# Optimization experiments

Hardware: AMD Instinct MI355X
Metric: run time of the kernel (lower is better)

The kernel has to match this reference:

```python
import jax, jax.numpy as jnp
import numpy as np

EPS = 2.220446049250313e-16  # np.finfo(float).eps, used by SparseDispatcher.combine


def setup_inputs() -> dict:
    key = jax.random.key(0)
    k1, k2, k3, k4, k5, k6 = jax.random.split(key, 6)
    N, D, H, E = 16384, 512, 2048, 8
    x = jax.random.normal(k1, (N, D), dtype=jnp.float32)
    w_gate = jax.random.normal(k2, (D, E), dtype=jnp.float32) * 0.05
    W1 = jax.random.normal(k3, (E - 1, D, H), dtype=jnp.float32) * 0.02
    b1 = jax.random.normal(k4, (E - 1, H), dtype=jnp.float32) * 0.02
    W2 = jax.random.normal(k5, (E - 1, H, D), dtype=jnp.float32) * 0.02
    b2 = jax.random.normal(k6, (E - 1, D), dtype=jnp.float32) * 0.02
    return {"x": x, "w_gate": w_gate, "W1": W1, "b1": b1, "W2": W2, "b2": b2, "k": 2}


def reference(x, w_gate, W1, b1, W2, b2, k):
    # --- top-k gating (input_choice, node-level, no noise / eval mode) ---
    N, E = x.shape[0], w_gate.shape[1]
    logits = x @ w_gate                                   # [N, E]
    top_vals, top_idx = jax.lax.top_k(logits, k)          # [N, k]
    top_gates = jax.nn.softmax(top_vals, axis=-1)         # softmax over selected experts
    gates = jnp.zeros((N, E), x.dtype).at[jnp.arange(N)[:, None], top_idx].set(top_gates)
    # --- dispatch / per-expert MLP / weighted combine ---
    # output[b] = sum_i gates[b,i] * expert_i(x[b]); last expert is identity.
    out = gates[:, E - 1 : E] * x                         # IdentityExpert (expert E-1)
    for e in range(W1.shape[0]):                          # fixed small expert count
        h = jax.nn.relu(x @ W1[e] + b1[e])                # [N, H]
        out = out + gates[:, e : e + 1] * (h @ W2[e] + b2[e])
    out = out.astype(jnp.float32)
    # combine() replaces exact zeros with machine epsilon
    return jnp.where(out == 0, EPS, out)
```

## Files before the change

### kernel.cpp

```cpp
#include <hip/hip_runtime.h>
#include <stdint.h>

#define EPS_VAL 2.220446049250313e-16f

typedef unsigned short u16;
typedef __bf16 bf16x8 __attribute__((ext_vector_type(8)));
typedef float f32x4 __attribute__((ext_vector_type(4)));

static __device__ __forceinline__ u16 f2bf(float v) {
    __bf16 b = (__bf16)v;
    return __builtin_bit_cast(u16, b);
}
static __device__ __forceinline__ float bf2f(u16 u) {
    __bf16 b = __builtin_bit_cast(__bf16, u);
    return (float)b;
}
static __device__ __forceinline__ void gll16(const void* g, void* l) {
    __builtin_amdgcn_global_load_lds(
        (const __attribute__((address_space(1))) unsigned int*)g,
        (__attribute__((address_space(3))) unsigned int*)l, 16, 0, 0);
}

#define MT_CAP 40

__global__ void k_transpose_cvt(const float* __restrict__ in, u16* __restrict__ out,
                                int R, int C) {
    __shared__ float t[32][33];
    const float* ip = in + (size_t)blockIdx.z * R * C;
    u16* op = out + (size_t)blockIdx.z * R * C;
    int tx = threadIdx.x & 31, ty = threadIdx.x >> 5;
    int c = blockIdx.x * 32 + tx;
    #pragma unroll
    for (int i = 0; i < 4; ++i) {
        int r = blockIdx.y * 32 + ty + i * 8;
        t[ty + i * 8][tx] = ip[(size_t)r * C + c];
    }
    __syncthreads();
    int r2 = blockIdx.y * 32 + tx;
    #pragma unroll
    for (int i = 0; i < 4; ++i) {
        int c2 = blockIdx.x * 32 + ty + i * 8;
        op[(size_t)c2 * R + r2] = f2bf(t[tx][ty + i * 8]);
    }
}

__global__ __launch_bounds__(1024) void k_gate(
    const float* __restrict__ x, const float* __restrict__ wg,
    u16* __restrict__ xb, int* __restrict__ cnt,
    uint2* __restrict__ asg, float4* __restrict__ rec) {
    __shared__ int hist[8];
    __shared__ int basep[8];
    __shared__ int   eA[64], eB[64], rA[64], rB[64];
    __shared__ float gA[64], gB[64];

    const int tid = threadIdx.x;
    if (tid < 8) hist[tid] = 0;
    __syncthreads();

    const int wv = tid >> 6, lane = tid & 63;
    #pragma unroll
    for (int it = 0; it < 4; ++it) {
        int rl  = it * 16 + wv;
        int row = blockIdx.x * 64 + rl;
        const float4* px = (const float4*)(x + (size_t)row * 512) + lane * 2;
        float4 v0 = px[0], v1 = px[1];
        union { u16 h[8]; uint4 u; } o;
        o.h[0]=f2bf(v0.x); o.h[1]=f2bf(v0.y); o.h[2]=f2bf(v0.z); o.h[3]=f2bf(v0.w);
        o.h[4]=f2bf(v1.x); o.h[5]=f2bf(v1.y); o.h[6]=f2bf(v1.z); o.h[7]=f2bf(v1.w);
        ((uint4*)(xb + (size_t)row * 512))[lane] = o.u;

        float xv[8] = {v0.x, v0.y, v0.z, v0.w, v1.x, v1.y, v1.z, v1.w};
        float a0=0,a1=0,a2=0,a3=0,a4=0,a5=0,a6=0,a7=0;
        const float4* wp = (const float4*)wg + (size_t)lane * 16;
        #pragma unroll
        for (int j = 0; j < 8; ++j) {
            float4 wa = wp[j * 2], wb = wp[j * 2 + 1];
            float v = xv[j];
            a0 += v*wa.x; a1 += v*wa.y; a2 += v*wa.z; a3 += v*wa.w;
            a4 += v*wb.x; a5 += v*wb.y; a6 += v*wb.z; a7 += v*wb.w;
        }
        #pragma unroll
        for (int off = 32; off; off >>= 1) {
            a0 += __shfl_xor(a0, off); a1 += __shfl_xor(a1, off);
            a2 += __shfl_xor(a2, off); a3 += __shfl_xor(a3, off);
            a4 += __shfl_xor(a4, off); a5 += __shfl_xor(a5, off);
            a6 += __shfl_xor(a6, off); a7 += __shfl_xor(a7, off);
        }
        if (lane == 0) {
            float v[8] = {a0,a1,a2,a3,a4,a5,a6,a7};
            int i0 = 0;
            #pragma unroll
            for (int e = 1; e < 8; ++e) if (v[e] > v[i0]) i0 = e;
            int i1 = (i0 == 0) ? 1 : 0;
            #pragma unroll
            for (int e = 0; e < 8; ++e) if (e != i0 && v[e] > v[i1]) i1 = e;
            float ex = expf(v[i1] - v[i0]);
            float g0 = 1.f / (1.f + ex), g1 = ex / (1.f + ex);
            rec[row] = make_float4(__int_as_float(i0), __int_as_float(i1), g0, g1);
            int r0 = (i0 != 7) ? atomicAdd(&hist[i0], 1) : -1;
            int r1 = (i1 != 7) ? atomicAdd(&hist[i1], 1) : -1;
            eA[rl] = i0; eB[rl] = i1; rA[rl] = r0; rB[rl] = r1;
            gA[rl] = g0; gB[rl] = g1;
        }
    }
    __syncthreads();
    if (tid < 7) basep[tid] = atomicAdd(&cnt[tid], hist[tid]);
    __syncthreads();
    if (tid < 64) {
        int row = blockIdx.x * 64 + tid;
        int i0 = eA[tid], i1 = eB[tid];
        if (i0 != 7)
            asg[i0 * 16384 + basep[i0] + rA[tid]] =
                make_uint2((unsigned)(row << 1), __float_as_uint(gA[tid]));
        if (i1 != 7)
            asg[i1 * 16384 + basep[i1] + rB[tid]] =
                make_uint2((unsigned)((row << 1) | 1), __float_as_uint(gB[tid]));
    }
}

__global__ void k_prefix(const int* __restrict__ cnt, int* __restrict__ off) {
    if (threadIdx.x == 0) {
        int s = 0;
        for (int e = 0; e < 7; ++e) { off[e] = s; s += cnt[e]; }
        off[7] = s;
    }
}

__global__ __launch_bounds__(256) void k_e1(
    const u16* __restrict__ xb, const u16* __restrict__ w1t,
    const float* __restrict__ b1, const int* __restrict__ cnt,
    const int* __restrict__ off, const uint2* __restrict__ asg,
    u16* __restrict__ Hb, int h0, int S, int NT)
{
    __shared__ __attribute__((aligned(16))) char smem[40960];

    const int bid = blockIdx.x;
    const int t   = (bid & 7) * (35 * NT) + (bid >> 3);
    const int e   = t / (MT_CAP * NT);
    const int rem = t - e * (MT_CAP * NT);
    const int mt  = rem / NT;
    const int nt  = rem - mt * NT;

    const int ce  = cnt[e];
    const int mtb = mt * 128;
    if (mtb >= ce) return;
    const int ntb = nt * 128;

    const int tid = threadIdx.x, wv = tid >> 6, lane = tid & 63;
    const int l16 = lane & 15, q = lane >> 4;
    const int wr = wv >> 1, wc = wv & 1;
    const u16* w1p = w1t + (size_t)e * 2048 * 512;

    const int nj = (wv < 2) ? 3 : 2;
    const u16* aS[3]; const u16* bS[3]; int js[3];
    #pragma unroll
    for (int jj = 0; jj < 3; ++jj) {
        int j = wv + jj * 4; js[jj] = j;
        if (j < 10) {
            int g = j * 64 + lane, row = g / 5, sl = g % 5;
            if (sl == 4) sl = 0;
            int idx = mtb + row;
            int rs = 0;
            if (idx < ce) rs = (int)asg[e * 16384 + idx].x >> 1;
            aS[jj] = xb + (size_t)rs * 512 + sl * 8;
            bS[jj] = w1p + (size_t)(h0 + ntb + row) * 512 + sl * 8;
        } else { aS[jj] = xb; bS[jj] = w1p; }
    }

    #pragma unroll
    for (int jj = 0; jj < 3; ++jj) if (jj < nj) {
        gll16(aS[jj], smem + js[jj] * 1024);
        gll16(bS[jj], smem + 20480 + js[jj] * 1024);
    }
    __syncthreads();

    f32x4 acc[4][4];
    #pragma unroll
    for (int mti = 0; mti < 4; ++mti)
        #pragma unroll
        for (int nti = 0; nti < 4; ++nti) acc[mti][nti] = (f32x4){0.f, 0.f, 0.f, 0.f};

    for (int kt = 0; kt < 16; ++kt) {
        const int cur = kt & 1;
        if (kt < 15) {
            char* An = smem + (cur ^ 1) * 10240;
            char* Bn = smem + 20480 + (cur ^ 1) * 10240;
            int ko = (kt + 1) * 32;
            #pragma unroll
            for (int jj = 0; jj < 3; ++jj) if (jj < nj) {
                gll16(aS[jj] + ko, An + js[jj] * 1024);
                gll16(bS[jj] + ko, Bn + js[jj] * 1024);
            }
        }
        const char* Ab = smem + cur * 10240;
        const char* Bb = smem + 20480 + cur * 10240;
        bf16x8 af[4], bf[4];
        #pragma unroll
        for (int mti = 0; mti < 4; ++mti)
            af[mti] = *(const bf16x8*)(Ab + (wr * 64 + mti * 16 + l16) * 80 + q * 16);
        #pragma unroll
        for (int nti = 0; nti < 4; ++nti)
            bf[nti] = *(const bf16x8*)(Bb + (wc * 64 + nti * 16 + l16) * 80 + q * 16);
        #pragma unroll
        for (int mti = 0; mti < 4; ++mti)
            #pragma unroll
            for (int nti = 0; nti < 4; ++nti)
                acc[mti][nti] = __builtin_amdgcn_mfma_f32_16x16x32_bf16(
                    af[mti], bf[nti], acc[mti][nti], 0, 0, 0);
        __syncthreads();
    }

    const size_t hbase = (size_t)off[e];
    #pragma unroll
    for (int nti = 0; nti < 4; ++nti) {
        int hcol = ntb + wc * 64 + nti * 16 + l16;
        float bias = b1[e * 2048 + h0 + hcol];
        #pragma unroll
        for (int mti = 0; mti < 4; ++mti) {
            #pragma unroll
            for (int r = 0; r < 4; ++r) {
                int i = mtb + wr * 64 + mti * 16 + q * 4 + r;
                if (i < ce) {
                    float v = acc[mti][nti][r] + bias;
                    v = v > 0.f ? v : 0.f;
                    Hb[(hbase + i) * S + hcol] = f2bf(v);
                }
            }
        }
    }
}

__global__ __launch_bounds__(256) void k_e2(
    const u16* __restrict__ Hb, const u16* __restrict__ w2t,
    const float* __restrict__ b2, const int* __restrict__ cnt,
    const int* __restrict__ off, const uint2* __restrict__ asg,
    u16* __restrict__ ybuf, int h0, int S, int firstPass, int lastPass)
{
    __shared__ __attribute__((aligned(16))) char smem[40960];

    const int bid = blockIdx.x;
    const int t   = (bid & 7) * 140 + (bid >> 3);
    const int e   = t / (MT_CAP * 4);
    const int rem = t - e * (MT_CAP * 4);
    const int mt  = rem >> 2;
    const int dt  = rem & 3;

    const int ce  = cnt[e];
    const int mtb = mt * 128;
    if (mtb >= ce) return;
    const int dtb = dt * 128;

    const int tid = threadIdx.x, wv = tid >> 6, lane = tid & 63;
    const int l16 = lane & 15, q = lane >> 4;
    const int wr = wv >> 1, wc = wv & 1;
    const u16* w2p = w2t + (size_t)e * 512 * 2048;
    const size_t hbase = (size_t)off[e];

    const int nj = (wv < 2) ? 3 : 2;
    const u16* aS[3]; const u16* bS[3]; int js[3];
    #pragma unroll
    for (int jj = 0; jj < 3; ++jj) {
        int j = wv + jj * 4; js[jj] = j;
        if (j < 10) {
            int g = j * 64 + lane, row = g / 5, sl = g % 5;
            if (sl == 4) sl = 0;
            aS[jj] = Hb + (hbase + mtb + row) * S + sl * 8;
            bS[jj] = w2p + (size_t)(dtb + row) * 2048 + h0 + sl * 8;
        } else { aS[jj] = Hb; bS[jj] = w2p; }
    }

    #pragma unroll
    for (int jj = 0; jj < 3; ++jj) if (jj < nj) {
        gll16(aS[jj], smem + js[jj] * 1024);
        gll16(bS[jj], smem + 20480 + js[jj] * 1024);
    }
    __syncthreads();

    f32x4 acc[4][4];
    #pragma unroll
    for (int mti = 0; mti < 4; ++mti)
        #pragma unroll
        for (int nti = 0; nti < 4; ++nti) acc[mti][nti] = (f32x4){0.f, 0.f, 0.f, 0.f};

    const int KT = S >> 5;
    for (int kt = 0; kt < KT; ++kt) {
        const int cur = kt & 1;
        if (kt + 1 < KT) {
            char* An = smem + (cur ^ 1) * 10240;
            char* Bn = smem + 20480 + (cur ^ 1) * 10240;
            int ko = (kt + 1) * 32;
            #pragma unroll
            for (int jj = 0; jj < 3; ++jj) if (jj < nj) {
                gll16(aS[jj] + ko, An + js[jj] * 1024);
                gll16(bS[jj] + ko, Bn + js[jj] * 1024);
            }
        }
        const char* Ab = smem + cur * 10240;
        const char* Bb = smem + 20480 + cur * 10240;
        bf16x8 af[4], bf[4];
        #pragma unroll
        for (int mti = 0; mti < 4; ++mti)
            af[mti] = *(const bf16x8*)(Ab + (wr * 64 + mti * 16 + l16) * 80 + q * 16);
        #pragma unroll
        for (int nti = 0; nti < 4; ++nti)
            bf[nti] = *(const bf16x8*)(Bb + (wc * 64 + nti * 16 + l16) * 80 + q * 16);
        #pragma unroll
        for (int mti = 0; mti < 4; ++mti)
            #pragma unroll
            for (int nti = 0; nti < 4; ++nti)
                acc[mti][nti] = __builtin_amdgcn_mfma_f32_16x16x32_bf16(
                    af[mti], bf[nti], acc[mti][nti], 0, 0, 0);
        __syncthreads();
    }

    #pragma unroll
    for (int nti = 0; nti < 4; ++nti) {
        int d = dtb + wc * 64 + nti * 16 + l16;
        float b2v = b2[e * 512 + d];
        #pragma unroll
        for (int mti = 0; mti < 4; ++mti) {
            #pragma unroll
            for (int r = 0; r < 4; ++r) {
                int lrow = wr * 64 + mti * 16 + q * 4 + r;
                int i = mtb + lrow;
                if (i < ce) {
                    uint2 a = asg[e * 16384 + i];
                    int rs = (int)a.x;
                    float g = __builtin_bit_cast(float, a.y);
                    float v = acc[mti][nti][r];
                    size_t yo = ((size_t)(rs & 1) * 16384 + (rs >> 1)) * 512 + d;
                    if (!firstPass) v += bf2f(ybuf[yo]);
                    if (lastPass)   v = g * (v + b2v);
                    ybuf[yo] = f2bf(v);
                }
            }
        }
    }
}

__global__ void k_final(const float* __restrict__ x, const float4* __restrict__ rec,
                        const u16* __restrict__ ybuf, float* __restrict__ out) {
    int i = blockIdx.x * 256 + threadIdx.x;
    int row = i >> 7;
    float4 r = rec[row];
    int e0 = __float_as_int(r.x), e1 = __float_as_int(r.y);
    float g7 = (e0 == 7) ? r.z : ((e1 == 7) ? r.w : 0.f);
    float4 xv = ((const float4*)x)[i];
    float o0 = g7 * xv.x, o1 = g7 * xv.y, o2 = g7 * xv.z, o3 = g7 * xv.w;
    size_t off = (size_t)i * 4;
    if (e0 != 7) {
        uint2 y = *(const uint2*)(ybuf + off);
        o0 += bf2f((u16)(y.x & 0xffff)); o1 += bf2f((u16)(y.x >> 16));
        o2 += bf2f((u16)(y.y & 0xffff)); o3 += bf2f((u16)(y.y >> 16));
    }
    if (e1 != 7) {
        uint2 y = *(const uint2*)(ybuf + 8388608 + off);
        o0 += bf2f((u16)(y.x & 0xffff)); o1 += bf2f((u16)(y.x >> 16));
        o2 += bf2f((u16)(y.y & 0xffff)); o3 += bf2f((u16)(y.y >> 16));
    }
    float4 res;
    res.x = (o0 == 0.f) ? EPS_VAL : o0;
    res.y = (o1 == 0.f) ? EPS_VAL : o1;
    res.z = (o2 == 0.f) ? EPS_VAL : o2;
    res.w = (o3 == 0.f) ? EPS_VAL : o3;
    ((float4*)out)[i] = res;
}

extern "C" void kernel_launch(void* const* d_in, const int* in_sizes, int n_in,
                              void* d_out, int out_size, void* d_ws, size_t ws_size,
                              hipStream_t stream) {
    const float* x  = (const float*)d_in[0];
    const float* wg = (const float*)d_in[1];
    const float* W1 = (const float*)d_in[2];
    const float* b1 = (const float*)d_in[3];
    const float* W2 = (const float*)d_in[4];
    const float* b2 = (const float*)d_in[5];
    (void)in_sizes; (void)n_in; (void)out_size;

    char* ws = (char*)d_ws;
    int*    cnt  = (int*)ws;
    int*    off  = (int*)(ws + 64);
    float4* rec  = (float4*)(ws + 256);
    uint2*  asg  = (uint2*)(ws + 262400);
    u16*    xb   = (u16*)(ws + 1179904);
    u16*    w1t  = (u16*)(ws + 17957120);
    u16*    w2t  = (u16*)(ws + 32637184);
    u16*    ybuf = (u16*)(ws + 47317248);
    u16*    Hb   = (u16*)(ws + 80871680);

    int S = 128;
    const int cands[4] = {2048, 1024, 512, 256};
    for (int c = 0; c < 4; ++c) {
        if (ws_size >= 80871680ull + (size_t)32896 * cands[c] * 2) { S = cands[c]; break; }
    }
    const int passes = 2048 / S;

    hipMemsetAsync(ws, 0, 256, stream);
    k_transpose_cvt<<<dim3(64, 16, 7), 256, 0, stream>>>(W1, w1t, 512, 2048);
    k_transpose_cvt<<<dim3(16, 64, 7), 256, 0, stream>>>(W2, w2t, 2048, 512);
    k_gate<<<256, 1024, 0, stream>>>(x, wg, xb, cnt, asg, rec);
    k_prefix<<<1, 64, 0, stream>>>(cnt, off);
    for (int p = 0; p < passes; ++p) {
        int h0 = p * S;
        int NT = S / 128;
        k_e1<<<7 * MT_CAP * NT, 256, 0, stream>>>(xb, w1t, b1, cnt, off, asg, Hb, h0, S, NT);
        k_e2<<<7 * MT_CAP * 4, 256, 0, stream>>>(Hb, w2t, b2, cnt, off, asg, ybuf,
                                                 h0, S, p == 0 ? 1 : 0,
                                                 p == passes - 1 ? 1 : 0);
    }
    k_final<<<8192, 256, 0, stream>>>(x, rec, ybuf, (float*)d_out);
}
```

Measured before the change: 340.2 us.

## Triple-buffer LDS tiles with explicit vmcnt waits in expert GEMMs

```diff
diff --git a/kernel.cpp b/kernel.cpp
--- a/kernel.cpp
+++ b/kernel.cpp
@@ -126,18 +126,19 @@
     }
 }
 
+
 __global__ __launch_bounds__(256) void k_e1(
     const u16* __restrict__ xb, const u16* __restrict__ w1t,
     const float* __restrict__ b1, const int* __restrict__ cnt,
     const int* __restrict__ off, const uint2* __restrict__ asg,
     u16* __restrict__ Hb, int h0, int S, int NT)
 {
-    __shared__ __attribute__((aligned(16))) char smem[40960];
+    __shared__ __attribute__((aligned(16))) char smem[61440];
 
     const int bid = blockIdx.x;
-    const int t   = (bid & 7) * (35 * NT) + (bid >> 3);
-    const int e   = t / (MT_CAP * NT);
-    const int rem = t - e * (MT_CAP * NT);
+    const int t0  = (bid & 7) * (35 * NT) + (bid >> 3);
+    const int e   = t0 / (MT_CAP * NT);
+    const int rem = t0 - e * (MT_CAP * NT);
     const int mt  = rem / NT;
     const int nt  = rem - mt * NT;
 
@@ -167,12 +168,23 @@
         } else { aS[jj] = xb; bS[jj] = w1p; }
     }
 
-    #pragma unroll
-    for (int jj = 0; jj < 3; ++jj) if (jj < nj) {
-        gll16(aS[jj], smem + js[jj] * 1024);
-        gll16(bS[jj], smem + 20480 + js[jj] * 1024);
-    }
-    __syncthreads();
+    auto ISSUE = [&](int b) {
+        char* An = smem + (b % 3) * 20480;
+        char* Bn = An + 10240;
+        int ko = b * 32;
+        #pragma unroll
+        for (int jj = 0; jj < 3; ++jj) if (jj < nj) {
+            gll16(aS[jj] + ko, An + js[jj] * 1024);
+            gll16(bS[jj] + ko, Bn + js[jj] * 1024);
+        }
+    };
+
+    ISSUE(0);
+    ISSUE(1);
+    if (wv < 2) asm volatile("s_waitcnt vmcnt(6) lgkmcnt(0)" ::: "memory");
+    else        asm volatile("s_waitcnt vmcnt(4) lgkmcnt(0)" ::: "memory");
+    __builtin_amdgcn_s_barrier();
+    __builtin_amdgcn_sched_barrier(0);
 
     f32x4 acc[4][4];
     #pragma unroll
@@ -180,20 +192,12 @@
         #pragma unroll
         for (int nti = 0; nti < 4; ++nti) acc[mti][nti] = (f32x4){0.f, 0.f, 0.f, 0.f};
 
-    for (int kt = 0; kt < 16; ++kt) {
-        const int cur = kt & 1;
-        if (kt < 15) {
-            char* An = smem + (cur ^ 1) * 10240;
-            char* Bn = smem + 20480 + (cur ^ 1) * 10240;
-            int ko = (kt + 1) * 32;
-            #pragma unroll
-            for (int jj = 0; jj < 3; ++jj) if (jj < nj) {
-                gll16(aS[jj] + ko, An + js[jj] * 1024);
-                gll16(bS[jj] + ko, Bn + js[jj] * 1024);
-            }
-        }
-        const char* Ab = smem + cur * 10240;
-        const char* Bb = smem + 20480 + cur * 10240;
+    const int KT = 16;
+    for (int t = 0; t < KT; ++t) {
+        if (t + 2 < KT) ISSUE(t + 2);
+
+        const char* Ab = smem + (t % 3) * 20480;
+        const char* Bb = Ab + 10240;
         bf16x8 af[4], bf[4];
         #pragma unroll
         for (int mti = 0; mti < 4; ++mti)
@@ -207,7 +211,17 @@
             for (int nti = 0; nti < 4; ++nti)
                 acc[mti][nti] = __builtin_amdgcn_mfma_f32_16x16x32_bf16(
                     af[mti], bf[nti], acc[mti][nti], 0, 0, 0);
-        __syncthreads();
+
+        if (t < KT - 1) {
+            if (t < KT - 2) {
+                if (wv < 2) asm volatile("s_waitcnt vmcnt(6) lgkmcnt(0)" ::: "memory");
+                else        asm volatile("s_waitcnt vmcnt(4) lgkmcnt(0)" ::: "memory");
+            } else {
+                asm volatile("s_waitcnt vmcnt(0) lgkmcnt(0)" ::: "memory");
+            }
+            __builtin_amdgcn_s_barrier();
+            __builtin_amdgcn_sched_barrier(0);
+        }
     }
 
     const size_t hbase = (size_t)off[e];
@@ -236,12 +250,12 @@
     const int* __restrict__ off, const uint2* __restrict__ asg,
     u16* __restrict__ ybuf, int h0, int S, int firstPass, int lastPass)
 {
-    __shared__ __attribute__((aligned(16))) char smem[40960];
+    __shared__ __attribute__((aligned(16))) char smem[61440];
 
     const int bid = blockIdx.x;
-    const int t   = (bid & 7) * 140 + (bid >> 3);
-    const int e   = t / (MT_CAP * 4);
-    const int rem = t - e * (MT_CAP * 4);
+    const int t0  = (bid & 7) * 140 + (bid >> 3);
+    const int e   = t0 / (MT_CAP * 4);
+    const int rem = t0 - e * (MT_CAP * 4);
     const int mt  = rem >> 2;
     const int dt  = rem & 3;
 
@@ -269,12 +283,23 @@
         } else { aS[jj] = Hb; bS[jj] = w2p; }
     }
 
-    #pragma unroll
-    for (int jj = 0; jj < 3; ++jj) if (jj < nj) {
-        gll16(aS[jj], smem + js[jj] * 1024);
-        gll16(bS[jj], smem + 20480 + js[jj] * 1024);
-    }
-    __syncthreads();
+    auto ISSUE = [&](int b) {
+        char* An = smem + (b % 3) * 20480;
+        char* Bn = An + 10240;
+        int ko = b * 32;
+        #pragma unroll
+        for (int jj = 0; jj < 3; ++jj) if (jj < nj) {
+            gll16(aS[jj] + ko, An + js[jj] * 1024);
+            gll16(bS[jj] + ko, Bn + js[jj] * 1024);
+        }
+    };
+
+    ISSUE(0);
+    ISSUE(1);
+    if (wv < 2) asm volatile("s_waitcnt vmcnt(6) lgkmcnt(0)" ::: "memory");
+    else        asm volatile("s_waitcnt vmcnt(4) lgkmcnt(0)" ::: "memory");
+    __builtin_amdgcn_s_barrier();
+    __builtin_amdgcn_sched_barrier(0);
 
     f32x4 acc[4][4];
     #pragma unroll
@@ -283,20 +308,11 @@
         for (int nti = 0; nti < 4; ++nti) acc[mti][nti] = (f32x4){0.f, 0.f, 0.f, 0.f};
 
     const int KT = S >> 5;
-    for (int kt = 0; kt < KT; ++kt) {
-        const int cur = kt & 1;
-        if (kt + 1 < KT) {
-            char* An = smem + (cur ^ 1) * 10240;
-            char* Bn = smem + 20480 + (cur ^ 1) * 10240;
-            int ko = (kt + 1) * 32;
-            #pragma unroll
-            for (int jj = 0; jj < 3; ++jj) if (jj < nj) {
-                gll16(aS[jj] + ko, An + js[jj] * 1024);
-                gll16(bS[jj] + ko, Bn + js[jj] * 1024);
-            }
-        }
-        const char* Ab = smem + cur * 10240;
-        const char* Bb = smem + 20480 + cur * 10240;
+    for (int t = 0; t < KT; ++t) {
+        if (t + 2 < KT) ISSUE(t + 2);
+
+        const char* Ab = smem + (t % 3) * 20480;
+        const char* Bb = Ab + 10240;
         bf16x8 af[4], bf[4];
         #pragma unroll
         for (int mti = 0; mti < 4; ++mti)
@@ -310,7 +326,17 @@
             for (int nti = 0; nti < 4; ++nti)
                 acc[mti][nti] = __builtin_amdgcn_mfma_f32_16x16x32_bf16(
                     af[mti], bf[nti], acc[mti][nti], 0, 0, 0);
-        __syncthreads();
+
+        if (t < KT - 1) {
+            if (t < KT - 2) {
+                if (wv < 2) asm volatile("s_waitcnt vmcnt(6) lgkmcnt(0)" ::: "memory");
+                else        asm volatile("s_waitcnt vmcnt(4) lgkmcnt(0)" ::: "memory");
+            } else {
+                asm volatile("s_waitcnt vmcnt(0) lgkmcnt(0)" ::: "memory");
+            }
+            __builtin_amdgcn_s_barrier();
+            __builtin_amdgcn_sched_barrier(0);
+        }
     }
 
     #pragma unroll
```

After: 370.9 us. +9.0%, slower.
